# Kernel optimization log

Hardware: AMD Instinct MI355X
Metric: run time of the kernel (lower is better)

## Reference

```python
import jax, jax.numpy as jnp
import numpy as np

B, S, D, H = 8, 2048, 768, 12

def setup_inputs() -> dict:
    key = jax.random.key(0)
    kx, km, kk, kq, kv = jax.random.split(key, 5)
    return {
        "x": jax.random.normal(kx, (B, S, D), dtype=jnp.float32),
        "mask": jax.random.randint(km, (B, 1, S), 0, 2, dtype=jnp.int32),
        "key_weight": jax.random.normal(kk, (D, H), dtype=jnp.float32),
        "query_weight": jax.random.normal(kq, (D, H), dtype=jnp.float32),
        "value_weight": jax.random.normal(kv, (D, H), dtype=jnp.float32),
    }

def reference(x, mask, key_weight, query_weight, value_weight):
    scale = 1.0 / (key_weight.shape[-1] ** 0.5)
    k = jnp.einsum('bsd,dh->bsh', x, key_weight)
    q = jnp.einsum('bsd,dh->bsh', x, query_weight)
    v = jnp.einsum('bsd,dh->bsh', x, value_weight)
    # scores: (B, S, T) — full score matrix as in the original
    scores = jnp.einsum('bsh,bth->bst', q, k) * scale
    scores = jnp.where(mask == 0, -jnp.inf, scores)
    attn = jax.nn.softmax(scores, axis=-1)
    return jnp.einsum('bst,bth->bsh', attn, v)
```

## Files before the change

### kernel.cpp

```cpp
#include <hip/hip_runtime.h>
#include <math.h>

#define QSCALE (0.2886751345948129f * 1.4426950408889634f)

#if __has_builtin(__builtin_amdgcn_exp2f)
#define EXP2F(x) __builtin_amdgcn_exp2f(x)
#else
#define EXP2F(x) exp2f(x)
#endif

typedef __attribute__((ext_vector_type(8))) _Float16 half8;
typedef __attribute__((ext_vector_type(4))) _Float16 half4_t;
typedef __attribute__((ext_vector_type(4))) float floatx4;

#define MFMA32F16(a, b, c) __builtin_amdgcn_mfma_f32_16x16x32_f16((a), (b), (c), 0, 0, 0)
#define MFMA16F16(a, b, c) __builtin_amdgcn_mfma_f32_16x16x16f16((a), (b), (c), 0, 0, 0)

static __device__ inline float bperm(float v, int addr_bytes) {
    return __int_as_float(__builtin_amdgcn_ds_bpermute(addr_bytes, __float_as_int(v)));
}

__global__ __launch_bounds__(256)
void prep(const float* __restrict__ Wq, const float* __restrict__ Wk,
          const float* __restrict__ Wv, const int* __restrict__ mask,
          _Float16* __restrict__ wfh, _Float16* __restrict__ wfl,
          int* __restrict__ dst, int* __restrict__ nvalid,
          float4* __restrict__ zbase)
{
    const int b = blockIdx.x;
    const int tid = threadIdx.x;
    if (b < 18) {
        int t = b * 256 + tid;
        if (t >= 4608) return;
        int lane = t & 63;
        int nt   = (t >> 6) % 3;
        int ks   = t / 192;
        const float* W = (nt == 0) ? Wq : (nt == 1) ? Wk : Wv;
        const float scale = (nt == 0) ? QSCALE : 1.0f;
        int col = lane & 15;
        int q8  = lane >> 4;
        half8 hi, lo;
        #pragma unroll
        for (int j = 0; j < 8; ++j) {
            int dim = ks * 32 + q8 * 8 + j;
            float f = (col < 12) ? W[dim * 12 + col] * scale : 0.0f;
            _Float16 h = (_Float16)f;
            hi[j] = h;
            lo[j] = (_Float16)(f - (float)h);
        }
        size_t off = ((size_t)(ks * 3 + nt) * 64 + lane) * 8;
        *(half8*)(wfh + off) = hi;
        *(half8*)(wfl + off) = lo;
    } else if (b < 26) {
        __shared__ int cnt[256];
        const int bb = b - 18;
        const int* mb = mask + bb * 2048;
        int local[8]; int c = 0;
        #pragma unroll
        for (int i = 0; i < 8; ++i) { local[i] = (mb[tid * 8 + i] != 0); c += local[i]; }
        cnt[tid] = c;
        __syncthreads();
        for (int off = 1; off < 256; off <<= 1) {
            int u = cnt[tid];
            int add = (tid >= off) ? cnt[tid - off] : 0;
            __syncthreads();
            cnt[tid] = u + add;
            __syncthreads();
        }
        int run = (tid == 0) ? 0 : cnt[tid - 1];
        int* db = dst + bb * 2048;
        #pragma unroll
        for (int i = 0; i < 8; ++i) { db[tid * 8 + i] = local[i] ? run : -1; run += local[i]; }
        if (tid == 255) nvalid[bb] = cnt[255];
    } else {
        const float4 z = make_float4(0.f, 0.f, 0.f, 0.f);
        for (int i = (b - 26) * 256 + tid; i < 163840; i += 38 * 256) zbase[i] = z;
    }
}

__global__ __launch_bounds__(256, 3)
void qkv_mfma(const float* __restrict__ x, const _Float16* __restrict__ wfh,
              const _Float16* __restrict__ wfl, const int* __restrict__ dst,
              _Float16* __restrict__ qA, _Float16* __restrict__ qB,
              _Float16* __restrict__ kfp, _Float16* __restrict__ vtf)
{
    __shared__ __align__(16) float cbuf[3072];
    const int tid  = threadIdx.x;
    const int lane = tid & 63;
    const int w    = tid >> 6;
    const int g    = blockIdx.x;
    const int rowbase = g * 16;
    const int m15 = lane & 15;
    const int q8  = lane >> 4;

    const float* xbase = x + (size_t)(rowbase + m15) * 768 + q8 * 8;
    const half8* WH = (const half8*)wfh;
    const half8* WL = (const half8*)wfl;

    float xv[6][8];
    #pragma unroll
    for (int s = 0; s < 6; ++s) {
        const int ks = w * 6 + s;
        *(float4*)(xv[s])     = *(const float4*)(xbase + ks * 32);
        *(float4*)(xv[s] + 4) = *(const float4*)(xbase + ks * 32 + 4);
    }

    floatx4 acc0 = {0.f, 0.f, 0.f, 0.f};
    floatx4 acc1 = acc0, acc2 = acc0;

    half8 bh[2][3], bl[2][3];
    {
        const int ks = w * 6;
        #pragma unroll
        for (int n = 0; n < 3; ++n) {
            bh[0][n] = WH[(ks * 3 + n) * 64 + lane];
            bl[0][n] = WL[(ks * 3 + n) * 64 + lane];
        }
    }

    #pragma unroll
    for (int s = 0; s < 6; ++s) {
        const int cur = s & 1, nxt = cur ^ 1;
        if (s < 5) {
            const int ksn = w * 6 + s + 1;
            #pragma unroll
            for (int n = 0; n < 3; ++n) {
                bh[nxt][n] = WH[(ksn * 3 + n) * 64 + lane];
                bl[nxt][n] = WL[(ksn * 3 + n) * 64 + lane];
            }
        }
        half8 ah, al;
        #pragma unroll
        for (int j = 0; j < 8; ++j) {
            _Float16 h = (_Float16)xv[s][j];
            ah[j] = h;
            al[j] = (_Float16)(xv[s][j] - (float)h);
        }
        acc0 = MFMA32F16(ah, bh[cur][0], acc0);
        acc1 = MFMA32F16(ah, bh[cur][1], acc1);
        acc2 = MFMA32F16(ah, bh[cur][2], acc2);
        acc0 = MFMA32F16(al, bh[cur][0], acc0);
        acc1 = MFMA32F16(al, bh[cur][1], acc1);
        acc2 = MFMA32F16(al, bh[cur][2], acc2);
        acc0 = MFMA32F16(ah, bl[cur][0], acc0);
        acc1 = MFMA32F16(ah, bl[cur][1], acc1);
        acc2 = MFMA32F16(ah, bl[cur][2], acc2);
    }

    *(floatx4*)(cbuf + ((w * 3 + 0) * 64 + lane) * 4) = acc0;
    *(floatx4*)(cbuf + ((w * 3 + 1) * 64 + lane) * 4) = acc1;
    *(floatx4*)(cbuf + ((w * 3 + 2) * 64 + lane) * 4) = acc2;
    __syncthreads();
    if (w < 3) {
        floatx4 t0 = *(const floatx4*)(cbuf + ((0 * 3 + w) * 64 + lane) * 4);
        floatx4 t1 = *(const floatx4*)(cbuf + ((1 * 3 + w) * 64 + lane) * 4);
        floatx4 t2 = *(const floatx4*)(cbuf + ((2 * 3 + w) * 64 + lane) * 4);
        floatx4 t3 = *(const floatx4*)(cbuf + ((3 * 3 + w) * 64 + lane) * 4);
        floatx4 tot = t0 + t1 + t2 + t3;
        const int col = m15;
        const int r0  = q8 * 4;
        #pragma unroll
        for (int r = 0; r < 4; ++r) {
            const int row = rowbase + r0 + r;
            const float val = tot[r];
            if (w == 0) {
                if (col < 12) {
                    size_t fb = (size_t)g * 64;
                    size_t offL = (fb + (col >> 3) * 16 + (r0 + r)) * 8 + (col & 7);
                    size_t offH = (fb + (2 + (col >> 3)) * 16 + (r0 + r)) * 8 + (col & 7);
                    _Float16 h = (_Float16)val;
                    qA[offL] = h;
                    qA[offH] = h;
                    qB[offL] = (_Float16)(val - (float)h);
                }
            } else {
                const int d = dst[row];
                if (d >= 0) {
                    const int bb = row >> 11;
                    if (w == 1) {
                        if (col < 12) {
                            size_t fb = ((size_t)(bb * 128 + (d >> 4))) * 64;
                            size_t offH = (fb + (col >> 3) * 16 + (d & 15)) * 8 + (col & 7);
                            size_t offL = (fb + (2 + (col >> 3)) * 16 + (d & 15)) * 8 + (col & 7);
                            _Float16 h = (_Float16)val;
                            kfp[offH] = h;
                            kfp[offL] = (_Float16)(val - (float)h);
                        }
                    } else {
                        if (col < 12) {
                            size_t off = (((size_t)(bb * 128 + (d >> 4))) * 64
                                          + ((d & 15) >> 2) * 16 + col) * 4 + (d & 3);
                            vtf[off] = (_Float16)val;
                        } else if (col == 12) {
                            size_t off = (((size_t)(bb * 128 + (d >> 4))) * 64
                                          + ((d & 15) >> 2) * 16 + 12) * 4 + (d & 3);
                            vtf[off] = (_Float16)1.0f;
                        }
                    }
                }
            }
        }
    }
}

__global__ __launch_bounds__(256)
void attn(const _Float16* __restrict__ qAf, const _Float16* __restrict__ qBf,
          const _Float16* __restrict__ kfp, const _Float16* __restrict__ vtf,
          const int* __restrict__ nvalid, float* __restrict__ out)
{
    __shared__ float cm[512];
    __shared__ __align__(16) floatx4 co[512];
    const int tid  = threadIdx.x;
    const int lane = tid & 63;
    const int w    = tid >> 6;
    const int bb   = blockIdx.x & 7;
    const int gl   = blockIdx.x >> 3;
    const int g0   = bb * 128 + gl * 2;
    const int m15  = lane & 15;

    const half8 qA0 = *(const half8*)(qAf + ((size_t)g0 * 64 + lane) * 8);
    const half8 qB0 = *(const half8*)(qBf + ((size_t)g0 * 64 + lane) * 8);
    const half8 qA1 = *(const half8*)(qAf + ((size_t)(g0 + 1) * 64 + lane) * 8);
    const half8 qB1 = *(const half8*)(qBf + ((size_t)(g0 + 1) * 64 + lane) * 8);

    const half8* KP = (const half8*)kfp + (size_t)bb * 128 * 64;
    const half4_t* VT = (const half4_t*)vtf + (size_t)bb * 128 * 64;

    const int nv = nvalid[bb];
    const int nt = (nv + 15) >> 4;
    const int a16 = (lane ^ 16) << 2;
    const int a32 = (lane ^ 32) << 2;

    float m0 = -INFINITY, m1 = -INFINITY;
    floatx4 o0 = {0.f, 0.f, 0.f, 0.f};
    floatx4 o1 = o0;

    int t = w;
    half8 kp;
    half4_t va;
    if (t < nt) {
        kp = KP[t * 64 + lane];
        va = VT[t * 64 + lane];
    }
    for (; t < nt; t += 4) {
        half8 nkp; half4_t nva;
        if (t + 4 < nt) {
            nkp = KP[(t + 4) * 64 + lane];
            nva = VT[(t + 4) * 64 + lane];
        }
        const floatx4 z = {0.f, 0.f, 0.f, 0.f};
        floatx4 s0a = MFMA32F16(kp, qA0, z);
        floatx4 s0b = MFMA32F16(kp, qB0, z);
        floatx4 s1a = MFMA32F16(kp, qA1, z);
        floatx4 s1b = MFMA32F16(kp, qB1, z);
        floatx4 s0 = s0a + s0b;
        floatx4 s1 = s1a + s1b;
        {
            float pm = fmaxf(fmaxf(s0.x, s0.y), fmaxf(s0.z, s0.w));
            pm = fmaxf(pm, bperm(pm, a16));
            pm = fmaxf(pm, bperm(pm, a32));
            half4_t pb;
            if (__all(pm <= m0)) {
                pb[0] = (_Float16)EXP2F(s0.x - m0);
                pb[1] = (_Float16)EXP2F(s0.y - m0);
                pb[2] = (_Float16)EXP2F(s0.z - m0);
                pb[3] = (_Float16)EXP2F(s0.w - m0);
            } else {
                float mnew = fmaxf(m0, pm);
                float corr = EXP2F(m0 - mnew);
                o0.x *= corr; o0.y *= corr; o0.z *= corr; o0.w *= corr;
                pb[0] = (_Float16)EXP2F(s0.x - mnew);
                pb[1] = (_Float16)EXP2F(s0.y - mnew);
                pb[2] = (_Float16)EXP2F(s0.z - mnew);
                pb[3] = (_Float16)EXP2F(s0.w - mnew);
                m0 = mnew;
            }
            o0 = MFMA16F16(va, pb, o0);
        }
        {
            float pm = fmaxf(fmaxf(s1.x, s1.y), fmaxf(s1.z, s1.w));
            pm = fmaxf(pm, bperm(pm, a16));
            pm = fmaxf(pm, bperm(pm, a32));
            half4_t pb;
            if (__all(pm <= m1)) {
                pb[0] = (_Float16)EXP2F(s1.x - m1);
                pb[1] = (_Float16)EXP2F(s1.y - m1);
                pb[2] = (_Float16)EXP2F(s1.z - m1);
                pb[3] = (_Float16)EXP2F(s1.w - m1);
            } else {
                float mnew = fmaxf(m1, pm);
                float corr = EXP2F(m1 - mnew);
                o1.x *= corr; o1.y *= corr; o1.z *= corr; o1.w *= corr;
                pb[0] = (_Float16)EXP2F(s1.x - mnew);
                pb[1] = (_Float16)EXP2F(s1.y - mnew);
                pb[2] = (_Float16)EXP2F(s1.z - mnew);
                pb[3] = (_Float16)EXP2F(s1.w - mnew);
                m1 = mnew;
            }
            o1 = MFMA16F16(va, pb, o1);
        }
        kp = nkp; va = nva;
    }

    cm[(0 * 4 + w) * 64 + lane] = m0;
    cm[(1 * 4 + w) * 64 + lane] = m1;
    co[(0 * 4 + w) * 64 + lane] = o0;
    co[(1 * 4 + w) * 64 + lane] = o1;
    __syncthreads();
    if (w < 2) {
        const int gi = w;
        float gm = -INFINITY;
        #pragma unroll
        for (int w2 = 0; w2 < 4; ++w2) gm = fmaxf(gm, cm[(gi * 4 + w2) * 64 + lane]);
        floatx4 O = {0.f, 0.f, 0.f, 0.f};
        #pragma unroll
        for (int w2 = 0; w2 < 4; ++w2) {
            float f = EXP2F(cm[(gi * 4 + w2) * 64 + lane] - gm);
            floatx4 ow = co[(gi * 4 + w2) * 64 + lane];
            O.x += ow.x * f; O.y += ow.y * f; O.z += ow.z * f; O.w += ow.w * f;
        }
        float L = bperm(O.x, (48 + m15) << 2);
        float inv = 1.0f / L;
        if ((lane >> 4) < 3) {
            float4 ov = make_float4(O.x * inv, O.y * inv, O.z * inv, O.w * inv);
            *(float4*)(out + ((size_t)(g0 + gi) * 16 + m15) * 12 + (lane >> 4) * 4) = ov;
        }
    }
}

extern "C" void kernel_launch(void* const* d_in, const int* in_sizes, int n_in,
                              void* d_out, int out_size, void* d_ws, size_t ws_size,
                              hipStream_t stream) {
    const float* x    = (const float*)d_in[0];
    const int*   mask = (const int*)  d_in[1];
    const float* Wk   = (const float*)d_in[2];
    const float* Wq   = (const float*)d_in[3];
    const float* Wv   = (const float*)d_in[4];
    float* out = (float*)d_out;

    char* base = (char*)d_ws;
    _Float16* qA  = (_Float16*)(base);
    _Float16* qB  = (_Float16*)(base + (1u << 20));
    _Float16* kfp = (_Float16*)(base + (2u << 20));
    _Float16* vtf = (_Float16*)(base + (3u << 20));
    _Float16* wfh = (_Float16*)(base + 3670016);
    _Float16* wfl = (_Float16*)(base + 3670016 + 73728);
    int* dst      = (int*)(base + 3817472);
    int* nvalid   = (int*)(base + 3817472 + 65536);
    float4* zbase = (float4*)(base + (1u << 20));

    prep<<<64, 256, 0, stream>>>(Wq, Wk, Wv, mask, wfh, wfl, dst, nvalid, zbase);
    qkv_mfma<<<1024, 256, 0, stream>>>(x, wfh, wfl, dst, qA, qB, kfp, vtf);
    attn<<<512, 256, 0, stream>>>(qA, qB, kfp, vtf, nvalid, out);
}
```

Measured before the change: 114.4 us.

## Fuse prep, QKV projection and attention into one cooperative kernel

Replaces the three separate launches (prep, qkv_mfma, attn) with a single cooperative kernel of 512 blocks that uses grid-wide syncs between the weight/mask prep, QKV projection and attention phases. The intent is to remove the launch overhead and inter-kernel gaps of three dispatches. The trade-off is the cost of two grid.sync barriers, a fixed grid of 512 blocks that must all be co-resident (two per CU via launch bounds), and projection work looping over 1024 row groups across those blocks. The old three-kernel path stays as a fallback if the cooperative launch fails.

```diff
diff --git a/kernel.cpp b/kernel.cpp
--- a/kernel.cpp
+++ b/kernel.cpp
@@ -1,5 +1,8 @@
 #include <hip/hip_runtime.h>
+#include <hip/hip_cooperative_groups.h>
 #include <math.h>
+
+namespace cg = cooperative_groups;
 
 #define QSCALE (0.2886751345948129f * 1.4426950408889634f)
 
@@ -18,6 +21,311 @@
 
 static __device__ inline float bperm(float v, int addr_bytes) {
     return __int_as_float(__builtin_amdgcn_ds_bpermute(addr_bytes, __float_as_int(v)));
+}
+
+__global__ __launch_bounds__(256, 2)
+void fused(const float* __restrict__ x, const int* __restrict__ mask,
+           const float* __restrict__ Wq, const float* __restrict__ Wk,
+           const float* __restrict__ Wv,
+           _Float16* __restrict__ wfh, _Float16* __restrict__ wfl,
+           int* __restrict__ dst, int* __restrict__ nvalid,
+           float4* __restrict__ zbase,
+           _Float16* __restrict__ qA, _Float16* __restrict__ qB,
+           _Float16* __restrict__ kfp, _Float16* __restrict__ vtf,
+           float* __restrict__ out)
+{
+    cg::grid_group grid = cg::this_grid();
+    __shared__ __align__(16) float smem_f[3072];
+    const int b    = blockIdx.x;
+    const int tid  = threadIdx.x;
+    const int lane = tid & 63;
+    const int w    = tid >> 6;
+    const int m15  = lane & 15;
+    const int q8   = lane >> 4;
+
+    if (b < 18) {
+        int t = b * 256 + tid;
+        if (t < 4608) {
+            int l2 = t & 63;
+            int wt = (t >> 6) % 3;
+            int ks = t / 192;
+            const float* W = (wt == 0) ? Wq : (wt == 1) ? Wk : Wv;
+            const float scale = (wt == 0) ? QSCALE : 1.0f;
+            int col = l2 & 15;
+            int qq  = l2 >> 4;
+            half8 hi, lo;
+            #pragma unroll
+            for (int j = 0; j < 8; ++j) {
+                int dim = ks * 32 + qq * 8 + j;
+                float f = (col < 12) ? W[dim * 12 + col] * scale : 0.0f;
+                _Float16 h = (_Float16)f;
+                hi[j] = h;
+                lo[j] = (_Float16)(f - (float)h);
+            }
+            size_t off = ((size_t)(ks * 3 + wt) * 64 + l2) * 8;
+            *(half8*)(wfh + off) = hi;
+            *(half8*)(wfl + off) = lo;
+        }
+    } else if (b < 26) {
+        int* cnt = (int*)smem_f;
+        const int bb = b - 18;
+        const int* mb = mask + bb * 2048;
+        int local[8]; int c = 0;
+        #pragma unroll
+        for (int i = 0; i < 8; ++i) { local[i] = (mb[tid * 8 + i] != 0); c += local[i]; }
+        cnt[tid] = c;
+        __syncthreads();
+        for (int off = 1; off < 256; off <<= 1) {
+            int u = cnt[tid];
+            int add = (tid >= off) ? cnt[tid - off] : 0;
+            __syncthreads();
+            cnt[tid] = u + add;
+            __syncthreads();
+        }
+        int run = (tid == 0) ? 0 : cnt[tid - 1];
+        int* db = dst + bb * 2048;
+        #pragma unroll
+        for (int i = 0; i < 8; ++i) { db[tid * 8 + i] = local[i] ? run : -1; run += local[i]; }
+        if (tid == 255) nvalid[bb] = cnt[255];
+    } else {
+        const float4 z = make_float4(0.f, 0.f, 0.f, 0.f);
+        for (int i = (b - 26) * 256 + tid; i < 163840; i += 486 * 256) zbase[i] = z;
+    }
+    grid.sync();
+
+    {
+        float* cbuf = smem_f;
+        const half8* WH = (const half8*)wfh;
+        const half8* WL = (const half8*)wfl;
+        for (int g = b; g < 1024; g += 512) {
+            const int rowbase = g * 16;
+            const float* xbase = x + (size_t)(rowbase + m15) * 768 + q8 * 8;
+
+            float xv[6][8];
+            #pragma unroll
+            for (int s = 0; s < 6; ++s) {
+                const int ks = w * 6 + s;
+                *(float4*)(xv[s])     = *(const float4*)(xbase + ks * 32);
+                *(float4*)(xv[s] + 4) = *(const float4*)(xbase + ks * 32 + 4);
+            }
+
+            floatx4 acc0 = {0.f, 0.f, 0.f, 0.f};
+            floatx4 acc1 = acc0, acc2 = acc0;
+
+            half8 bh[2][3], bl[2][3];
+            {
+                const int ks = w * 6;
+                #pragma unroll
+                for (int n = 0; n < 3; ++n) {
+                    bh[0][n] = WH[(ks * 3 + n) * 64 + lane];
+                    bl[0][n] = WL[(ks * 3 + n) * 64 + lane];
+                }
+            }
+
+            #pragma unroll
+            for (int s = 0; s < 6; ++s) {
+                const int cur = s & 1, nxt = cur ^ 1;
+                if (s < 5) {
+                    const int ksn = w * 6 + s + 1;
+                    #pragma unroll
+                    for (int n = 0; n < 3; ++n) {
+                        bh[nxt][n] = WH[(ksn * 3 + n) * 64 + lane];
+                        bl[nxt][n] = WL[(ksn * 3 + n) * 64 + lane];
+                    }
+                }
+                half8 ah, al;
+                #pragma unroll
+                for (int j = 0; j < 8; ++j) {
+                    _Float16 h = (_Float16)xv[s][j];
+                    ah[j] = h;
+                    al[j] = (_Float16)(xv[s][j] - (float)h);
+                }
+                acc0 = MFMA32F16(ah, bh[cur][0], acc0);
+                acc1 = MFMA32F16(ah, bh[cur][1], acc1);
+                acc2 = MFMA32F16(ah, bh[cur][2], acc2);
+                acc0 = MFMA32F16(al, bh[cur][0], acc0);
+                acc1 = MFMA32F16(al, bh[cur][1], acc1);
+                acc2 = MFMA32F16(al, bh[cur][2], acc2);
+                acc0 = MFMA32F16(ah, bl[cur][0], acc0);
+                acc1 = MFMA32F16(ah, bl[cur][1], acc1);
+                acc2 = MFMA32F16(ah, bl[cur][2], acc2);
+            }
+
+            *(floatx4*)(cbuf + ((w * 3 + 0) * 64 + lane) * 4) = acc0;
+            *(floatx4*)(cbuf + ((w * 3 + 1) * 64 + lane) * 4) = acc1;
+            *(floatx4*)(cbuf + ((w * 3 + 2) * 64 + lane) * 4) = acc2;
+            __syncthreads();
+            if (w < 3) {
+                floatx4 t0 = *(const floatx4*)(cbuf + ((0 * 3 + w) * 64 + lane) * 4);
+                floatx4 t1 = *(const floatx4*)(cbuf + ((1 * 3 + w) * 64 + lane) * 4);
+                floatx4 t2 = *(const floatx4*)(cbuf + ((2 * 3 + w) * 64 + lane) * 4);
+                floatx4 t3 = *(const floatx4*)(cbuf + ((3 * 3 + w) * 64 + lane) * 4);
+                floatx4 tot = t0 + t1 + t2 + t3;
+                const int col = m15;
+                const int r0  = q8 * 4;
+                #pragma unroll
+                for (int r = 0; r < 4; ++r) {
+                    const int row = rowbase + r0 + r;
+                    const float val = tot[r];
+                    if (w == 0) {
+                        if (col < 12) {
+                            size_t fb = (size_t)g * 64;
+                            size_t offL = (fb + (col >> 3) * 16 + (r0 + r)) * 8 + (col & 7);
+                            size_t offH = (fb + (2 + (col >> 3)) * 16 + (r0 + r)) * 8 + (col & 7);
+                            _Float16 h = (_Float16)val;
+                            qA[offL] = h;
+                            qA[offH] = h;
+                            qB[offL] = (_Float16)(val - (float)h);
+                        }
+                    } else {
+                        const int d = dst[row];
+                        if (d >= 0) {
+                            const int bb = row >> 11;
+                            if (w == 1) {
+                                if (col < 12) {
+                                    size_t fb = ((size_t)(bb * 128 + (d >> 4))) * 64;
+                                    size_t offH = (fb + (col >> 3) * 16 + (d & 15)) * 8 + (col & 7);
+                                    size_t offL = (fb + (2 + (col >> 3)) * 16 + (d & 15)) * 8 + (col & 7);
+                                    _Float16 h = (_Float16)val;
+                                    kfp[offH] = h;
+                                    kfp[offL] = (_Float16)(val - (float)h);
+                                }
+                            } else {
+                                if (col < 12) {
+                                    size_t off = (((size_t)(bb * 128 + (d >> 4))) * 64
+                                                  + ((d & 15) >> 2) * 16 + col) * 4 + (d & 3);
+                                    vtf[off] = (_Float16)val;
+                                } else if (col == 12) {
+                                    size_t off = (((size_t)(bb * 128 + (d >> 4))) * 64
+                                                  + ((d & 15) >> 2) * 16 + 12) * 4 + (d & 3);
+                                    vtf[off] = (_Float16)1.0f;
+                                }
+                            }
+                        }
+                    }
+                }
+            }
+            __syncthreads();
+        }
+    }
+    grid.sync();
+
+    {
+        float* cm = smem_f;
+        floatx4* co = (floatx4*)(smem_f + 512);
+        const int bb = b & 7;
+        const int gl = b >> 3;
+        const int g0 = bb * 128 + gl * 2;
+
+        const half8 qA0 = *(const half8*)(qA + ((size_t)g0 * 64 + lane) * 8);
+        const half8 qB0 = *(const half8*)(qB + ((size_t)g0 * 64 + lane) * 8);
+        const half8 qA1 = *(const half8*)(qA + ((size_t)(g0 + 1) * 64 + lane) * 8);
+        const half8 qB1 = *(const half8*)(qB + ((size_t)(g0 + 1) * 64 + lane) * 8);
+
+        const half8* KP = (const half8*)kfp + (size_t)bb * 128 * 64;
+        const half4_t* VT = (const half4_t*)vtf + (size_t)bb * 128 * 64;
+
+        const int nv = nvalid[bb];
+        const int ntk = (nv + 15) >> 4;
+        const int a16 = (lane ^ 16) << 2;
+        const int a32 = (lane ^ 32) << 2;
+
+        float m0 = -INFINITY, m1 = -INFINITY;
+        floatx4 o0 = {0.f, 0.f, 0.f, 0.f};
+        floatx4 o1 = o0;
+
+        int t = w;
+        half8 kp;
+        half4_t va;
+        if (t < ntk) {
+            kp = KP[t * 64 + lane];
+            va = VT[t * 64 + lane];
+        }
+        for (; t < ntk; t += 4) {
+            half8 nkp; half4_t nva;
+            if (t + 4 < ntk) {
+                nkp = KP[(t + 4) * 64 + lane];
+                nva = VT[(t + 4) * 64 + lane];
+            }
+            const floatx4 z = {0.f, 0.f, 0.f, 0.f};
+            floatx4 s0a = MFMA32F16(kp, qA0, z);
+            floatx4 s0b = MFMA32F16(kp, qB0, z);
+            floatx4 s1a = MFMA32F16(kp, qA1, z);
+            floatx4 s1b = MFMA32F16(kp, qB1, z);
+            floatx4 s0 = s0a + s0b;
+            floatx4 s1 = s1a + s1b;
+            {
+                float pm = fmaxf(fmaxf(s0.x, s0.y), fmaxf(s0.z, s0.w));
+                pm = fmaxf(pm, bperm(pm, a16));
+                pm = fmaxf(pm, bperm(pm, a32));
+                half4_t pb;
+                if (__all(pm <= m0)) {
+                    pb[0] = (_Float16)EXP2F(s0.x - m0);
+                    pb[1] = (_Float16)EXP2F(s0.y - m0);
+                    pb[2] = (_Float16)EXP2F(s0.z - m0);
+                    pb[3] = (_Float16)EXP2F(s0.w - m0);
+                } else {
+                    float mnew = fmaxf(m0, pm);
+                    float corr = EXP2F(m0 - mnew);
+                    o0.x *= corr; o0.y *= corr; o0.z *= corr; o0.w *= corr;
+                    pb[0] = (_Float16)EXP2F(s0.x - mnew);
+                    pb[1] = (_Float16)EXP2F(s0.y - mnew);
+                    pb[2] = (_Float16)EXP2F(s0.z - mnew);
+                    pb[3] = (_Float16)EXP2F(s0.w - mnew);
+                    m0 = mnew;
+                }
+                o0 = MFMA16F16(va, pb, o0);
+            }
+            {
+                float pm = fmaxf(fmaxf(s1.x, s1.y), fmaxf(s1.z, s1.w));
+                pm = fmaxf(pm, bperm(pm, a16));
+                pm = fmaxf(pm, bperm(pm, a32));
+                half4_t pb;
+                if (__all(pm <= m1)) {
+                    pb[0] = (_Float16)EXP2F(s1.x - m1);
+                    pb[1] = (_Float16)EXP2F(s1.y - m1);
+                    pb[2] = (_Float16)EXP2F(s1.z - m1);
+                    pb[3] = (_Float16)EXP2F(s1.w - m1);
+                } else {
+                    float mnew = fmaxf(m1, pm);
+                    float corr = EXP2F(m1 - mnew);
+                    o1.x *= corr; o1.y *= corr; o1.z *= corr; o1.w *= corr;
+                    pb[0] = (_Float16)EXP2F(s1.x - mnew);
+                    pb[1] = (_Float16)EXP2F(s1.y - mnew);
+                    pb[2] = (_Float16)EXP2F(s1.z - mnew);
+                    pb[3] = (_Float16)EXP2F(s1.w - mnew);
+                    m1 = mnew;
+                }
+                o1 = MFMA16F16(va, pb, o1);
+            }
+            kp = nkp; va = nva;
+        }
+
+        cm[(0 * 4 + w) * 64 + lane] = m0;
+        cm[(1 * 4 + w) * 64 + lane] = m1;
+        co[(0 * 4 + w) * 64 + lane] = o0;
+        co[(1 * 4 + w) * 64 + lane] = o1;
+        __syncthreads();
+        if (w < 2) {
+            const int gi = w;
+            float gm = -INFINITY;
+            #pragma unroll
+            for (int w2 = 0; w2 < 4; ++w2) gm = fmaxf(gm, cm[(gi * 4 + w2) * 64 + lane]);
+            floatx4 O = {0.f, 0.f, 0.f, 0.f};
+            #pragma unroll
+            for (int w2 = 0; w2 < 4; ++w2) {
+                float f = EXP2F(cm[(gi * 4 + w2) * 64 + lane] - gm);
+                floatx4 ow = co[(gi * 4 + w2) * 64 + lane];
+                O.x += ow.x * f; O.y += ow.y * f; O.z += ow.z * f; O.w += ow.w * f;
+            }
+            float L = bperm(O.x, (48 + m15) << 2);
+            float inv = 1.0f / L;
+            if ((lane >> 4) < 3) {
+                float4 ov = make_float4(O.x * inv, O.y * inv, O.z * inv, O.w * inv);
+                *(float4*)(out + ((size_t)(g0 + gi) * 16 + m15) * 12 + (lane >> 4) * 4) = ov;
+            }
+        }
+    }
 }
 
 __global__ __launch_bounds__(256)
@@ -349,7 +657,15 @@
     int* nvalid   = (int*)(base + 3817472 + 65536);
     float4* zbase = (float4*)(base + (1u << 20));
 
-    prep<<<64, 256, 0, stream>>>(Wq, Wk, Wv, mask, wfh, wfl, dst, nvalid, zbase);
-    qkv_mfma<<<1024, 256, 0, stream>>>(x, wfh, wfl, dst, qA, qB, kfp, vtf);
-    attn<<<512, 256, 0, stream>>>(qA, qB, kfp, vtf, nvalid, out);
+    void* args[] = { (void*)&x, (void*)&mask, (void*)&Wq, (void*)&Wk, (void*)&Wv,
+                     (void*)&wfh, (void*)&wfl, (void*)&dst, (void*)&nvalid,
+                     (void*)&zbase, (void*)&qA, (void*)&qB, (void*)&kfp,
+                     (void*)&vtf, (void*)&out };
+    hipError_t err = hipLaunchCooperativeKernel((const void*)fused, dim3(512),
+                                                dim3(256), args, 0, stream);
+    if (err != hipSuccess) {
+        prep<<<64, 256, 0, stream>>>(Wq, Wk, Wv, mask, wfh, wfl, dst, nvalid, zbase);
+        qkv_mfma<<<1024, 256, 0, stream>>>(x, wfh, wfl, dst, qA, qB, kfp, vtf);
+        attn<<<512, 256, 0, stream>>>(qA, qB, kfp, vtf, nvalid, out);
+    }
 }
```

Result: slower. 235.2 us (+105.6%).
